# Kernel tuning notes

Measured on AMD Instinct MI355X. Metric: run time of the kernel, lower is better.

Reference implementation:

```python
import jax, jax.numpy as jnp
import numpy as np

B, S, DIM, H = 2, 2048, 1024, 16
HD = DIM // H  # head dim = 64


def setup_inputs() -> dict:
    key = jax.random.key(0)
    ks = jax.random.split(key, 10)
    scale = 1.0 / np.sqrt(DIM)
    x = jax.random.normal(ks[0], (B, S, DIM), dtype=jnp.float32)
    # per-head projection weights stacked over heads: [H, DIM, HD]
    Wq = jax.random.normal(ks[1], (H, DIM, HD), dtype=jnp.float32) * scale
    bq = jax.random.normal(ks[2], (H, HD), dtype=jnp.float32) * 0.01
    Wk = jax.random.normal(ks[3], (H, DIM, HD), dtype=jnp.float32) * scale
    bk = jax.random.normal(ks[4], (H, HD), dtype=jnp.float32) * 0.01
    Wv = jax.random.normal(ks[5], (H, DIM, HD), dtype=jnp.float32) * scale
    bv = jax.random.normal(ks[6], (H, HD), dtype=jnp.float32) * 0.01
    # output linear: [DIM, DIM]
    Wo = jax.random.normal(ks[7], (DIM, DIM), dtype=jnp.float32) * scale
    bo = jax.random.normal(ks[8], (DIM,), dtype=jnp.float32) * 0.01
    return {"x": x, "Wq": Wq, "bq": bq, "Wk": Wk, "bk": bk,
            "Wv": Wv, "bv": bv, "Wo": Wo, "bo": bo}


def reference(x, Wq, bq, Wk, bk, Wv, bv, Wo, bo):
    # per-head projections: [B, H, S, HD]
    q = jnp.einsum('bsd,hde->bhse', x, Wq) + bq[None, :, None, :]
    k = jnp.einsum('bsd,hde->bhse', x, Wk) + bk[None, :, None, :]
    v = jnp.einsum('bsd,hde->bhse', x, Wv) + bv[None, :, None, :]
    # causal attention scores: [B, H, S, S], scaled by sqrt(head_dim)
    scores = jnp.einsum('bhse,bhte->bhst', q, k) / jnp.sqrt(jnp.float32(HD))
    causal = jnp.tril(jnp.ones((S, S), dtype=bool))
    scores = jnp.where(causal[None, None], scores, -jnp.inf)
    attn = jax.nn.softmax(scores, axis=-1)
    out = jnp.einsum('bhst,bhte->bhse', attn, v)  # [B, H, S, HD]
    # concat heads in order -> [B, S, DIM]
    out = out.transpose(0, 2, 1, 3).reshape(B, S, DIM)
    return out @ Wo + bo
```

## Files before the change

kernel.cpp:

```cpp
#include <hip/hip_runtime.h>

typedef _Float16 half8 __attribute__((ext_vector_type(8)));
typedef _Float16 half4 __attribute__((ext_vector_type(4)));
typedef float f32x4 __attribute__((ext_vector_type(4)));

#define MFMA32(a, b, c) __builtin_amdgcn_mfma_f32_16x16x32_f16((a), (b), (c), 0, 0, 0)
#define MFMA16(a, b, c) __builtin_amdgcn_mfma_f32_16x16x16f16((a), (b), (c), 0, 0, 0)

static constexpr int Bc = 2, Sc = 2048, DIMc = 1024, Hc = 16, HDc = 64;
static constexpr int Mc = Bc * Sc;
static constexpr int NQKV = 3 * DIMc;

__device__ __forceinline__ void gl_lds16(const _Float16* g, _Float16* l) {
  __builtin_amdgcn_global_load_lds(
      (const __attribute__((address_space(1))) void*)g,
      (__attribute__((address_space(3))) void*)l, 16, 0, 0);
}


__global__ __launch_bounds__(256) void k_prep_all(
    const float* __restrict__ x, const float* __restrict__ Wq,
    const float* __restrict__ Wk, const float* __restrict__ Wv,
    const float* __restrict__ Wo, _Float16* __restrict__ xh,
    _Float16* __restrict__ WallT, _Float16* __restrict__ WoT) {
  __shared__ float Ls[64 * 65];
  const int bx = blockIdx.x, tid = threadIdx.x;
  if (bx < 16384) {
    int i = bx * 256 + tid;
    xh[i] = (_Float16)x[i];
    return;
  }
  int b2 = bx - 16384;
  if (b2 < 768) {
    const int dt = b2 & 15, ph = b2 >> 4;
    const int p = ph >> 4, h = ph & 15;
    const float* W = (p == 0) ? Wq : (p == 1) ? Wk : Wv;
    for (int c = tid; c < 4096; c += 256) {
      int dr = c >> 6, e = c & 63;
      Ls[e * 65 + dr] = W[h * 65536 + (dt * 64 + dr) * 64 + e];
    }
    __syncthreads();
    for (int c = tid; c < 4096; c += 256) {
      int e = c >> 6, dr = c & 63;
      WallT[(size_t)(p * 1024 + h * 64 + e) * 1024 + dt * 64 + dr] = (_Float16)Ls[e * 65 + dr];
    }
  } else {
    int b3 = b2 - 768;
    const int dt = b3 & 15, nt = b3 >> 4;
    for (int c = tid; c < 4096; c += 256) {
      int dr = c >> 6, nl = c & 63;
      Ls[nl * 65 + dr] = Wo[(dt * 64 + dr) * 1024 + nt * 64 + nl];
    }
    __syncthreads();
    for (int c = tid; c < 4096; c += 256) {
      int nl = c >> 6, dr = c & 63;
      WoT[(size_t)(nt * 64 + nl) * 1024 + dt * 64 + dr] = (_Float16)Ls[nl * 65 + dr];
    }
  }
}


#define GEMM_CORE()                                                            \
  __shared__ _Float16 As[128 * 64];                                            \
  __shared__ _Float16 Bs[128 * 64];                                            \
  const int tid = threadIdx.x;                                                 \
  const int lane = tid & 63, wave = tid >> 6;                                  \
  const int quad = lane >> 4, mr = lane & 15, m7 = mr & 7;                     \
  const int wm = wave >> 1, wn = wave & 1;                                     \
  f32x4 acc[4][4];                                                             \
  for (int i = 0; i < 4; i++)                                                  \
    for (int j = 0; j < 4; j++) acc[i][j] = f32x4{0.f, 0.f, 0.f, 0.f};         \
  for (int k0 = 0; k0 < DIMc; k0 += 64) {                                      \
    __syncthreads();                                                           \
    for (int it = 0; it < 4; ++it) {                                           \
      int idx = it * 256 + tid;                                                \
      int row = idx >> 3, scb = (idx & 7) ^ (row & 7);                         \
      gl_lds16(&A[(size_t)(m0 + row) * DIMc + k0 + scb * 8],                   \
               &As[(it * 256 + wave * 64) * 8]);                               \
    }                                                                          \
    for (int it = 0; it < 4; ++it) {                                           \
      int idx = it * 256 + tid;                                                \
      int row = idx >> 3, scb = (idx & 7) ^ (row & 7);                         \
      gl_lds16(&Bt[(size_t)(n0 + row) * DIMc + k0 + scb * 8],                  \
               &Bs[(it * 256 + wave * 64) * 8]);                               \
    }                                                                          \
    __syncthreads();                                                           \
    for (int kk = 0; kk < 2; ++kk) {                                           \
      half8 af[4], bf[4];                                                      \
      for (int i = 0; i < 4; i++)                                              \
        af[i] = *(const half8*)&As[(wm * 64 + i * 16 + mr) * 64 +              \
                                   (((kk * 4 + quad) ^ m7) * 8)];              \
      for (int i = 0; i < 4; i++)                                              \
        bf[i] = *(const half8*)&Bs[(wn * 64 + i * 16 + mr) * 64 +              \
                                   (((kk * 4 + quad) ^ m7) * 8)];              \
      for (int i = 0; i < 4; i++)                                              \
        for (int j = 0; j < 4; j++) acc[i][j] = MFMA32(af[i], bf[j], acc[i][j]); \
    }                                                                          \
  }

__global__ __launch_bounds__(256) void k_gemm_qkv(
    const _Float16* __restrict__ xh, const _Float16* __restrict__ WallT,
    const float* __restrict__ bq, const float* __restrict__ bk,
    const float* __restrict__ bv, _Float16* __restrict__ qh,
    _Float16* __restrict__ kh, _Float16* __restrict__ vT) {
  const int id = blockIdx.x;
  const bool qkrole = id < 512;
  const _Float16* A;
  const _Float16* Bt;
  int m0, n0;
  if (qkrole) {
    A = xh; Bt = WallT;
    n0 = (id & 15) * 128; m0 = (id >> 4) * 128;
  } else {
    int j = id - 512;
    A = WallT + (size_t)2048 * DIMc; Bt = xh;
    n0 = (j & 31) * 128; m0 = (j >> 5) * 128;
  }
  GEMM_CORE()
  if (qkrole) {
    for (int i = 0; i < 4; i++) {
      for (int j = 0; j < 4; j++) {
        int col = n0 + wn * 64 + j * 16 + mr;
        int p = col >> 10, rem = col & 1023;
        const float* bias = p ? bk : bq;
        _Float16* dst = p ? kh : qh;
        float bb = bias[rem];
        int h = rem >> 6, e = rem & 63;
        for (int r = 0; r < 4; r++) {
          int row = m0 + wm * 64 + i * 16 + quad * 4 + r;
          int b = row >> 11, s = row & 2047;
          dst[(((size_t)(b * Hc + h)) * Sc + s) * HDc + e] = (_Float16)(acc[i][j][r] + bb);
        }
      }
    }
  } else {
    for (int i = 0; i < 4; i++) {
      int rowb = m0 + wm * 64 + i * 16 + quad * 4;
      for (int j = 0; j < 4; j++) {
        int col = n0 + wn * 64 + j * 16 + mr;
        int b = col >> 11, s = col & 2047;
        for (int r = 0; r < 4; r++) {
          int row = rowb + r;
          vT[(size_t)(b * 1024 + row) * Sc + s] = (_Float16)(acc[i][j][r] + bv[row]);
        }
      }
    }
  }
}

__global__ __launch_bounds__(256) void k_gemm_out(
    const _Float16* __restrict__ A, const _Float16* __restrict__ Bt,
    const float* __restrict__ bo, float* __restrict__ out) {
  const int m0 = blockIdx.y * 128, n0 = blockIdx.x * 128;
  GEMM_CORE()
  for (int i = 0; i < 4; i++) {
    for (int j = 0; j < 4; j++) {
      int col = n0 + wn * 64 + j * 16 + mr;
      float bb = bo[col];
      for (int r = 0; r < 4; r++) {
        int row = m0 + wm * 64 + i * 16 + quad * 4 + r;
        out[(size_t)row * DIMc + col] = acc[i][j][r] + bb;
      }
    }
  }
}


__global__ __launch_bounds__(128, 2) void k_attn(
    const _Float16* __restrict__ qg, const _Float16* __restrict__ kg,
    const _Float16* __restrict__ vTg, _Float16* __restrict__ att) {
  const int xb = blockIdx.x;
  const int qt = (xb & 1) ? (xb >> 1) : (31 - (xb >> 1));
  const int bh = blockIdx.y;
  const int b = bh >> 4, h = bh & 15;
  const int tid = threadIdx.x, wave = tid >> 6, lane = tid & 63;
  const int quad = lane >> 4, mr = lane & 15, m7 = mr & 7;
  const size_t base = (size_t)bh * (Sc * HDc);
  const size_t vbase = ((size_t)b * 1024 + h * 64) * Sc;

  __shared__ _Float16 Ks[2][64 * 64];
  __shared__ _Float16 Vt[2][64 * 64];

  const int q0 = qt * 64 + wave * 32;

  const _Float16 qsc = (_Float16)(0.125f * 1.44269504f);
  half8 aq[2][2];
  for (int qf = 0; qf < 2; ++qf)
    for (int c = 0; c < 2; ++c) {
      half8 v = *(const half8*)&qg[base + (size_t)(q0 + qf * 16 + mr) * 64 + c * 32 + quad * 8];
      for (int j = 0; j < 8; ++j) v[j] = v[j] * qsc;
      aq[qf][c] = v;
    }

  f32x4 o[4][2], ol[2];
  for (int nf = 0; nf < 4; ++nf)
    for (int qf = 0; qf < 2; ++qf) o[nf][qf] = f32x4{0.f, 0.f, 0.f, 0.f};
  ol[0] = ol[1] = f32x4{0.f, 0.f, 0.f, 0.f};
  const half4 ones = {(_Float16)1.f, (_Float16)1.f, (_Float16)1.f, (_Float16)1.f};

  const int nt = qt + 1;

  for (int it = 0; it < 4; ++it) {
    int idx = it * 128 + tid;
    int row = idx >> 3, scb = (idx & 7) ^ (row & 7);
    gl_lds16(kg + base + (size_t)row * 64 + scb * 8, &Ks[0][(it * 128 + wave * 64) * 8]);
  }
  for (int it = 0; it < 4; ++it) {
    int idx = it * 128 + tid;
    int row = idx >> 3, scb = (idx & 7) ^ (row & 7);
    gl_lds16(vTg + vbase + (size_t)row * Sc + scb * 8, &Vt[0][(it * 128 + wave * 64) * 8]);
  }
  __syncthreads();

  for (int t = 0; t < nt; ++t) {
    const int cur = t & 1;
    if (t + 1 < nt) {
      const int nxt = cur ^ 1;
      const _Float16* ks = kg + base + (size_t)(t + 1) * (64 * 64);
      const _Float16* vs = vTg + vbase + (t + 1) * 64;
      for (int it = 0; it < 4; ++it) {
        int idx = it * 128 + tid;
        int row = idx >> 3, scb = (idx & 7) ^ (row & 7);
        gl_lds16(ks + (size_t)row * 64 + scb * 8, &Ks[nxt][(it * 128 + wave * 64) * 8]);
      }
      for (int it = 0; it < 4; ++it) {
        int idx = it * 128 + tid;
        int row = idx >> 3, scb = (idx & 7) ^ (row & 7);
        gl_lds16(vs + (size_t)row * Sc + scb * 8, &Vt[nxt][(it * 128 + wave * 64) * 8]);
      }
    }

    f32x4 sf[2][4];
    for (int kf = 0; kf < 4; ++kf) {
      const int r0 = (kf * 16 + mr) * 64;
      half8 k0 = *(const half8*)&Ks[cur][r0 + ((quad ^ m7) * 8)];
      half8 k1 = *(const half8*)&Ks[cur][r0 + (((quad ^ 4) ^ m7) * 8)];
      for (int qf = 0; qf < 2; ++qf) {
        f32x4 z = {0.f, 0.f, 0.f, 0.f};
        z = MFMA32(k0, aq[qf][0], z);
        z = MFMA32(k1, aq[qf][1], z);
        sf[qf][kf] = z;
      }
    }

    const bool diag = (t == qt);
    half4 pf[2][4];
    for (int qf = 0; qf < 2; ++qf) {
      const int q = q0 + qf * 16 + mr;
      for (int kf = 0; kf < 4; ++kf) {
        half4 pp;
        const int kvb = t * 64 + kf * 16 + quad * 4;
        for (int r = 0; r < 4; ++r) {
          float p = __builtin_amdgcn_exp2f(sf[qf][kf][r]);
          if (diag && (kvb + r > q)) p = 0.f;
          pp[r] = (_Float16)p;
        }
        pf[qf][kf] = pp;
      }
    }

    for (int nf = 0; nf < 4; ++nf) {
      const int er = (nf * 16 + mr) * 64;
      for (int kc = 0; kc < 4; ++kc) {
        int kb = kc * 2 + (quad >> 1);
        half4 vv = *(const half4*)&Vt[cur][er + ((kb ^ m7) * 8) + (quad & 1) * 4];
        for (int qf = 0; qf < 2; ++qf) o[nf][qf] = MFMA16(vv, pf[qf][kc], o[nf][qf]);
      }
    }
    for (int kc = 0; kc < 4; ++kc)
      for (int qf = 0; qf < 2; ++qf) ol[qf] = MFMA16(ones, pf[qf][kc], ol[qf]);

    __syncthreads();
  }

  for (int qf = 0; qf < 2; ++qf) {
    const float inv = 1.0f / ol[qf][0];
    const int q = q0 + qf * 16 + mr;
    for (int nf = 0; nf < 4; ++nf) {
      half4 ov;
      for (int r = 0; r < 4; ++r) ov[r] = (_Float16)(o[nf][qf][r] * inv);
      *(half4*)&att[((size_t)(b * Sc + q)) * DIMc + h * 64 + nf * 16 + quad * 4] = ov;
    }
  }
}


extern "C" void kernel_launch(void* const* d_in, const int* in_sizes, int n_in,
                              void* d_out, int out_size, void* d_ws, size_t ws_size,
                              hipStream_t stream) {
  const float* x  = (const float*)d_in[0];
  const float* Wq = (const float*)d_in[1];
  const float* bq = (const float*)d_in[2];
  const float* Wk = (const float*)d_in[3];
  const float* bk = (const float*)d_in[4];
  const float* Wv = (const float*)d_in[5];
  const float* bv = (const float*)d_in[6];
  const float* Wo = (const float*)d_in[7];
  const float* bo = (const float*)d_in[8];
  float* out = (float*)d_out;

  _Float16* p = (_Float16*)d_ws;
  _Float16* xh    = p; p += (size_t)Mc * DIMc;
  _Float16* WallT = p; p += (size_t)NQKV * DIMc;
  _Float16* WoT   = p; p += (size_t)DIMc * DIMc;
  _Float16* qh    = p; p += (size_t)Bc * Hc * Sc * HDc;
  _Float16* kh    = p; p += (size_t)Bc * Hc * Sc * HDc;
  _Float16* vT    = p; p += (size_t)Bc * Hc * Sc * HDc;
  _Float16* atth  = p;

  k_prep_all<<<16384 + 768 + 256, 256, 0, stream>>>(x, Wq, Wk, Wv, Wo, xh, WallT, WoT);
  k_gemm_qkv<<<768, 256, 0, stream>>>(xh, WallT, bq, bk, bv, qh, kh, vT);
  k_attn<<<dim3(32, Bc * Hc), 128, 0, stream>>>(qh, kh, vT, atth);
  k_gemm_out<<<dim3(DIMc / 128, Mc / 128), 256, 0, stream>>>(atth, WoT, bo, out);
}
```

Before: 218.8 us.

## Split KV tiles across four waves per query tile with LDS reduction

The attention kernel now gives each 256-thread block one 64-row query tile. The four waves each take every fourth KV tile, with their own double-buffered LDS staging and only per-wave vmcnt waits, so no block-wide barriers run inside the loop. Partial outputs and row sums are reduced through shared memory at the end. The grid becomes 1D and is ordered longest tiles first. The aim is to remove per-iteration __syncthreads, raise parallelism within a query tile, and balance the causal workload. In exchange the block uses a large LDS footprint (128 KB plus the reduction buffer), adds a reduction epilogue, and the waves within a block carry uneven loads.

```diff
diff --git a/kernel.cpp b/kernel.cpp
--- a/kernel.cpp
+++ b/kernel.cpp
@@ -166,93 +166,93 @@
 }
 
 
-__global__ __launch_bounds__(128, 2) void k_attn(
+__global__ __launch_bounds__(256, 1) void k_attn(
     const _Float16* __restrict__ qg, const _Float16* __restrict__ kg,
     const _Float16* __restrict__ vTg, _Float16* __restrict__ att) {
-  const int xb = blockIdx.x;
-  const int qt = (xb & 1) ? (xb >> 1) : (31 - (xb >> 1));
-  const int bh = blockIdx.y;
+  const int bid = blockIdx.x;
+  const int qt = 31 - (bid >> 5);
+  const int bh = bid & 31;
   const int b = bh >> 4, h = bh & 15;
-  const int tid = threadIdx.x, wave = tid >> 6, lane = tid & 63;
+  const int tid = threadIdx.x, w = tid >> 6, lane = tid & 63;
   const int quad = lane >> 4, mr = lane & 15, m7 = mr & 7;
   const size_t base = (size_t)bh * (Sc * HDc);
   const size_t vbase = ((size_t)b * 1024 + h * 64) * Sc;
 
-  __shared__ _Float16 Ks[2][64 * 64];
-  __shared__ _Float16 Vt[2][64 * 64];
-
-  const int q0 = qt * 64 + wave * 32;
+  __shared__ _Float16 KV[4][2][2][64 * 64];
+  __shared__ float Lsh[4][64];
+
+  const int q0 = qt * 64;
+  const int myn = (qt >= w) ? ((qt - w) >> 2) + 1 : 0;
 
   const _Float16 qsc = (_Float16)(0.125f * 1.44269504f);
-  half8 aq[2][2];
-  for (int qf = 0; qf < 2; ++qf)
+  half8 aq[4][2];
+  for (int qf = 0; qf < 4; ++qf)
     for (int c = 0; c < 2; ++c) {
       half8 v = *(const half8*)&qg[base + (size_t)(q0 + qf * 16 + mr) * 64 + c * 32 + quad * 8];
       for (int j = 0; j < 8; ++j) v[j] = v[j] * qsc;
       aq[qf][c] = v;
     }
 
-  f32x4 o[4][2], ol[2];
+  f32x4 o[4][4];
+  f32x4 ol[4];
   for (int nf = 0; nf < 4; ++nf)
-    for (int qf = 0; qf < 2; ++qf) o[nf][qf] = f32x4{0.f, 0.f, 0.f, 0.f};
-  ol[0] = ol[1] = f32x4{0.f, 0.f, 0.f, 0.f};
+    for (int qf = 0; qf < 4; ++qf) o[nf][qf] = f32x4{0.f, 0.f, 0.f, 0.f};
+  for (int qf = 0; qf < 4; ++qf) ol[qf] = f32x4{0.f, 0.f, 0.f, 0.f};
   const half4 ones = {(_Float16)1.f, (_Float16)1.f, (_Float16)1.f, (_Float16)1.f};
 
-  const int nt = qt + 1;
-
-  for (int it = 0; it < 4; ++it) {
-    int idx = it * 128 + tid;
-    int row = idx >> 3, scb = (idx & 7) ^ (row & 7);
-    gl_lds16(kg + base + (size_t)row * 64 + scb * 8, &Ks[0][(it * 128 + wave * 64) * 8]);
-  }
-  for (int it = 0; it < 4; ++it) {
-    int idx = it * 128 + tid;
-    int row = idx >> 3, scb = (idx & 7) ^ (row & 7);
-    gl_lds16(vTg + vbase + (size_t)row * Sc + scb * 8, &Vt[0][(it * 128 + wave * 64) * 8]);
-  }
-  __syncthreads();
-
-  for (int t = 0; t < nt; ++t) {
-    const int cur = t & 1;
-    if (t + 1 < nt) {
-      const int nxt = cur ^ 1;
-      const _Float16* ks = kg + base + (size_t)(t + 1) * (64 * 64);
-      const _Float16* vs = vTg + vbase + (t + 1) * 64;
-      for (int it = 0; it < 4; ++it) {
-        int idx = it * 128 + tid;
+  if (myn > 0) {
+    const _Float16* ks = kg + base + (size_t)w * 4096;
+    const _Float16* vs = vTg + vbase + w * 64;
+    for (int it = 0; it < 8; ++it) {
+      int idx = it * 64 + lane;
+      int row = idx >> 3, scb = (idx & 7) ^ (row & 7);
+      gl_lds16(ks + (size_t)row * 64 + scb * 8, &KV[w][0][0][it * 512]);
+    }
+    for (int it = 0; it < 8; ++it) {
+      int idx = it * 64 + lane;
+      int row = idx >> 3, scb = (idx & 7) ^ (row & 7);
+      gl_lds16(vs + (size_t)row * Sc + scb * 8, &KV[w][0][1][it * 512]);
+    }
+  }
+  asm volatile("s_waitcnt vmcnt(0)" ::: "memory");
+
+  for (int i = 0; i < myn; ++i) {
+    const int t = w + (i << 2);
+    const _Float16* Kc = &KV[w][i & 1][0][0];
+    const _Float16* Vc = &KV[w][i & 1][1][0];
+
+    if (i + 1 < myn) {
+      const _Float16* ks = kg + base + (size_t)(t + 4) * 4096;
+      const _Float16* vs = vTg + vbase + (t + 4) * 64;
+      _Float16* Kn = &KV[w][(i + 1) & 1][0][0];
+      _Float16* Vn = &KV[w][(i + 1) & 1][1][0];
+      for (int it = 0; it < 8; ++it) {
+        int idx = it * 64 + lane;
         int row = idx >> 3, scb = (idx & 7) ^ (row & 7);
-        gl_lds16(ks + (size_t)row * 64 + scb * 8, &Ks[nxt][(it * 128 + wave * 64) * 8]);
-      }
-      for (int it = 0; it < 4; ++it) {
-        int idx = it * 128 + tid;
+        gl_lds16(ks + (size_t)row * 64 + scb * 8, Kn + it * 512);
+      }
+      for (int it = 0; it < 8; ++it) {
+        int idx = it * 64 + lane;
         int row = idx >> 3, scb = (idx & 7) ^ (row & 7);
-        gl_lds16(vs + (size_t)row * Sc + scb * 8, &Vt[nxt][(it * 128 + wave * 64) * 8]);
-      }
-    }
-
-    f32x4 sf[2][4];
+        gl_lds16(vs + (size_t)row * Sc + scb * 8, Vn + it * 512);
+      }
+    }
+
+    const bool diag = (t == qt);
+    half4 pf[4][4];
     for (int kf = 0; kf < 4; ++kf) {
       const int r0 = (kf * 16 + mr) * 64;
-      half8 k0 = *(const half8*)&Ks[cur][r0 + ((quad ^ m7) * 8)];
-      half8 k1 = *(const half8*)&Ks[cur][r0 + (((quad ^ 4) ^ m7) * 8)];
-      for (int qf = 0; qf < 2; ++qf) {
+      half8 k0 = *(const half8*)&Kc[r0 + ((quad ^ m7) * 8)];
+      half8 k1 = *(const half8*)&Kc[r0 + (((quad ^ 4) ^ m7) * 8)];
+      for (int qf = 0; qf < 4; ++qf) {
         f32x4 z = {0.f, 0.f, 0.f, 0.f};
         z = MFMA32(k0, aq[qf][0], z);
         z = MFMA32(k1, aq[qf][1], z);
-        sf[qf][kf] = z;
-      }
-    }
-
-    const bool diag = (t == qt);
-    half4 pf[2][4];
-    for (int qf = 0; qf < 2; ++qf) {
-      const int q = q0 + qf * 16 + mr;
-      for (int kf = 0; kf < 4; ++kf) {
         half4 pp;
-        const int kvb = t * 64 + kf * 16 + quad * 4;
+        const int kvb = kf * 16 + quad * 4;
         for (int r = 0; r < 4; ++r) {
-          float p = __builtin_amdgcn_exp2f(sf[qf][kf][r]);
-          if (diag && (kvb + r > q)) p = 0.f;
+          float p = __builtin_amdgcn_exp2f(z[r]);
+          if (diag && (kvb + r > qf * 16 + mr)) p = 0.f;
           pp[r] = (_Float16)p;
         }
         pf[qf][kf] = pp;
@@ -263,25 +263,42 @@
       const int er = (nf * 16 + mr) * 64;
       for (int kc = 0; kc < 4; ++kc) {
         int kb = kc * 2 + (quad >> 1);
-        half4 vv = *(const half4*)&Vt[cur][er + ((kb ^ m7) * 8) + (quad & 1) * 4];
-        for (int qf = 0; qf < 2; ++qf) o[nf][qf] = MFMA16(vv, pf[qf][kc], o[nf][qf]);
+        half4 vv = *(const half4*)&Vc[er + ((kb ^ m7) * 8) + (quad & 1) * 4];
+        for (int qf = 0; qf < 4; ++qf) o[nf][qf] = MFMA16(vv, pf[qf][kc], o[nf][qf]);
       }
     }
     for (int kc = 0; kc < 4; ++kc)
-      for (int qf = 0; qf < 2; ++qf) ol[qf] = MFMA16(ones, pf[qf][kc], ol[qf]);
-
-    __syncthreads();
-  }
-
-  for (int qf = 0; qf < 2; ++qf) {
-    const float inv = 1.0f / ol[qf][0];
-    const int q = q0 + qf * 16 + mr;
-    for (int nf = 0; nf < 4; ++nf) {
-      half4 ov;
-      for (int r = 0; r < 4; ++r) ov[r] = (_Float16)(o[nf][qf][r] * inv);
-      *(half4*)&att[((size_t)(b * Sc + q)) * DIMc + h * 64 + nf * 16 + quad * 4] = ov;
-    }
-  }
+      for (int qf = 0; qf < 4; ++qf) ol[qf] = MFMA16(ones, pf[qf][kc], ol[qf]);
+
+    asm volatile("s_waitcnt vmcnt(0)" ::: "memory");
+  }
+
+  __syncthreads();
+  float* Osh = (float*)&KV[0][0][0][0];
+  for (int nf = 0; nf < 4; ++nf)
+    for (int qf = 0; qf < 4; ++qf)
+      for (int r = 0; r < 4; ++r)
+        Osh[w * 4096 + (nf * 16 + quad * 4 + r) * 64 + qf * 16 + mr] = o[nf][qf][r];
+  if (quad == 0)
+    for (int qf = 0; qf < 4; ++qf) Lsh[w][qf * 16 + mr] = ol[qf][0];
+  __syncthreads();
+
+  const int q = tid & 63, e0 = (tid >> 6) * 16;
+  const float linv = 1.0f / (Lsh[0][q] + Lsh[1][q] + Lsh[2][q] + Lsh[3][q]);
+  half8 o0, o1;
+  for (int e = 0; e < 8; ++e) {
+    float s = Osh[(e0 + e) * 64 + q] + Osh[4096 + (e0 + e) * 64 + q] +
+              Osh[8192 + (e0 + e) * 64 + q] + Osh[12288 + (e0 + e) * 64 + q];
+    o0[e] = (_Float16)(s * linv);
+  }
+  for (int e = 8; e < 16; ++e) {
+    float s = Osh[(e0 + e) * 64 + q] + Osh[4096 + (e0 + e) * 64 + q] +
+              Osh[8192 + (e0 + e) * 64 + q] + Osh[12288 + (e0 + e) * 64 + q];
+    o1[e - 8] = (_Float16)(s * linv);
+  }
+  const size_t orow = ((size_t)(b * Sc + q0 + q)) * DIMc + h * 64 + e0;
+  *(half8*)&att[orow] = o0;
+  *(half8*)&att[orow + 8] = o1;
 }
 
 
@@ -310,6 +327,6 @@
 
   k_prep_all<<<16384 + 768 + 256, 256, 0, stream>>>(x, Wq, Wk, Wv, Wo, xh, WallT, WoT);
   k_gemm_qkv<<<768, 256, 0, stream>>>(xh, WallT, bq, bk, bv, qh, kh, vT);
-  k_attn<<<dim3(32, Bc * Hc), 128, 0, stream>>>(qh, kh, vT, atth);
+  k_attn<<<1024, 256, 0, stream>>>(qh, kh, vT, atth);
   k_gemm_out<<<dim3(DIMc / 128, Mc / 128), 256, 0, stream>>>(atth, WoT, bo, out);
 }
```

Result: faster. 212.3 us (-3.0%).
